# Performance work log

Hardware: AMD Instinct MI355X
Metric: run time of the kernel (lower is better)

Reference implementation:

```python
import jax, jax.numpy as jnp
import numpy as np

BETA = 0.25            # commitment loss weight
ENT_RATIO = 0.1        # entropy regularization weight
ENT_TEMP = 0.01        # entropy loss temperature
EPS = 1e-5


def setup_inputs() -> dict:
    key = jax.random.key(0)
    k1, k2 = jax.random.split(key)
    z = jax.random.normal(k1, (32, 8, 16, 16), dtype=jnp.float32)       # [B, e_dim, H, W]
    codebook = jax.random.normal(k2, (16384, 8), dtype=jnp.float32)     # [K, e_dim]
    return {"z": z, "codebook": codebook}


def _entropy_loss(affinity):
    # affinity: [N, K] = -distances; torch divides by temperature in-place
    flat = affinity / ENT_TEMP
    probs = jax.nn.softmax(flat, axis=-1)
    log_probs = jax.nn.log_softmax(flat + EPS, axis=-1)
    avg_probs = jnp.mean(probs, axis=0)                                  # [K]
    avg_entropy = -jnp.sum(avg_probs * jnp.log(avg_probs + EPS))
    sample_entropy = -jnp.mean(jnp.sum(probs * log_probs, axis=-1))
    return sample_entropy - avg_entropy


def reference(z, codebook):
    B, C, H, W = z.shape
    sg = jax.lax.stop_gradient
    # [B,C,H,W] -> [N, e_dim]
    zf = jnp.transpose(z, (0, 2, 3, 1)).reshape(-1, C)
    # squared euclidean distances: ||z||^2 + ||e||^2 - 2 z e^T  -> [N, K]
    d = (jnp.sum(zf * zf, axis=1, keepdims=True)
         + jnp.sum(codebook * codebook, axis=1)[None, :]
         - 2.0 * jnp.einsum('nd,kd->nk', zf, codebook))
    idx = jnp.argmin(d, axis=1)                                          # [N]
    zq_f = codebook[idx]                                                 # [N, e_dim] gather
    # VQ losses (codebook + beta * commitment) and entropy regularization
    vq_loss = jnp.mean((zq_f - sg(zf)) ** 2)
    commit_loss = BETA * jnp.mean((sg(zq_f) - zf) ** 2)
    ent_loss = ENT_RATIO * _entropy_loss(-d)
    loss = vq_loss + commit_loss + ent_loss
    # straight-through estimator
    zq_f = zf + sg(zq_f - zf)
    z_q = jnp.transpose(zq_f.reshape(B, H, W, C), (0, 3, 1, 2))
    return z_q, loss, idx.reshape(B, H, W)
```

## Files before the change

kernel.cpp:

```cpp
#include <hip/hip_runtime.h>
#include <math.h>


#define KCODES 16384
#define CAP 192

__device__ __forceinline__ float dot8s(const float (&z)[8], float4 c0,
                                       float4 c1, float b) {
    float a = fmaf(z[0], c0.x, b);
    a = fmaf(z[1], c0.y, a);
    a = fmaf(z[2], c0.z, a);
    a = fmaf(z[3], c0.w, a);
    a = fmaf(z[4], c1.x, a);
    a = fmaf(z[5], c1.y, a);
    a = fmaf(z[6], c1.z, a);
    a = fmaf(z[7], c1.w, a);
    return a;
}

__global__ __launch_bounds__(256) void prep_cb(const float* __restrict__ cb,
                                               float* __restrict__ bk,
                                               float* __restrict__ avgp,
                                               int* __restrict__ flag,
                                               float* __restrict__ scal) {
    int k = blockIdx.x * 256 + threadIdx.x;
    const float4* c4 = (const float4*)cb;
    float4 c0 = c4[2 * k], c1 = c4[2 * k + 1];
    float nrm = c0.x * c0.x + c0.y * c0.y + c0.z * c0.z + c0.w * c0.w
              + c1.x * c1.x + c1.y * c1.y + c1.z * c1.z + c1.w * c1.w;
    bk[k] = -100.0f * nrm;
    avgp[k] = 0.0f;
    if (k < 8192) flag[k] = 0;
    if (k < 8)    scal[k] = 0.0f;
}

__global__ __launch_bounds__(256, 2) void pass1(
    const float* __restrict__ z, const float* __restrict__ cb,
    const float* __restrict__ bk, float* __restrict__ mrow,
    int* __restrict__ flag, float* __restrict__ out_zq,
    float* __restrict__ out_idx, float* __restrict__ scal,
    float* __restrict__ avgp)
{
    __shared__ float wfb[16][CAP];
    __shared__ int   wkb[16][CAP];
    __shared__ int   cnt[16];
    __shared__ float redSq[4], redEnt[4];

    const int wave = threadIdx.x >> 6;
    const int lane = threadIdx.x & 63;
    const int w4 = wave * 4;
    const int row0 = blockIdx.x * 16 + w4;

    float zr[4][8];
#pragma unroll
    for (int r = 0; r < 4; ++r) {
        int row = row0 + r;
        const float* p = z + (row >> 8) * 2048 + (row & 255);
#pragma unroll
        for (int c = 0; c < 8; ++c) zr[r][c] = 200.0f * p[c * 256];
    }
    if (lane < 4) cnt[w4 + lane] = 0;
    __syncthreads();

    const float4* c4 = (const float4*)cb;
    float m[4], mt[4];
#pragma unroll
    for (int r = 0; r < 4; ++r) m[r] = -3.4e38f;

#pragma unroll
    for (int j = 0; j < 8; ++j) {
        int k = lane + 64 * j;
        float4 c0 = c4[2 * k], c1 = c4[2 * k + 1];
        float b = bk[k];
#pragma unroll
        for (int r = 0; r < 4; ++r) m[r] = fmaxf(m[r], dot8s(zr[r], c0, c1, b));
    }
#pragma unroll
    for (int off = 32; off; off >>= 1) {
#pragma unroll
        for (int r = 0; r < 4; ++r) m[r] = fmaxf(m[r], __shfl_xor(m[r], off));
    }
#pragma unroll
    for (int r = 0; r < 4; ++r) mt[r] = m[r] - 87.0f;

    float4 A0[4], A1[4]; float Ab[4];
    float4 B0[4], B1[4]; float Bb[4];

    auto loadA = [&](int bat) {
#pragma unroll
        for (int jj = 0; jj < 4; ++jj) {
            int k = lane + bat * 256 + 64 * jj;
            A0[jj] = c4[2 * k]; A1[jj] = c4[2 * k + 1]; Ab[jj] = bk[k];
        }
    };
    auto loadB = [&](int bat) {
#pragma unroll
        for (int jj = 0; jj < 4; ++jj) {
            int k = lane + bat * 256 + 64 * jj;
            B0[jj] = c4[2 * k]; B1[jj] = c4[2 * k + 1]; Bb[jj] = bk[k];
        }
    };
    auto comp = [&](int bat, const float4 (&P0)[4], const float4 (&P1)[4],
                    const float (&PB)[4]) {
#pragma unroll
        for (int jj = 0; jj < 4; ++jj) {
            float f0 = dot8s(zr[0], P0[jj], P1[jj], PB[jj]);
            float f1 = dot8s(zr[1], P0[jj], P1[jj], PB[jj]);
            float f2 = dot8s(zr[2], P0[jj], P1[jj], PB[jj]);
            float f3 = dot8s(zr[3], P0[jj], P1[jj], PB[jj]);
            bool h0 = f0 > mt[0], h1 = f1 > mt[1];
            bool h2 = f2 > mt[2], h3 = f3 > mt[3];
            if (__any(h0 | h1 | h2 | h3)) {
                int k = lane + bat * 256 + 64 * jj;
                if (h0) { m[0] = fmaxf(m[0], f0); mt[0] = m[0] - 87.0f;
                    int s_ = atomicAdd(&cnt[w4 + 0], 1);
                    if (s_ < CAP) { wfb[w4 + 0][s_] = f0; wkb[w4 + 0][s_] = k; } }
                if (h1) { m[1] = fmaxf(m[1], f1); mt[1] = m[1] - 87.0f;
                    int s_ = atomicAdd(&cnt[w4 + 1], 1);
                    if (s_ < CAP) { wfb[w4 + 1][s_] = f1; wkb[w4 + 1][s_] = k; } }
                if (h2) { m[2] = fmaxf(m[2], f2); mt[2] = m[2] - 87.0f;
                    int s_ = atomicAdd(&cnt[w4 + 2], 1);
                    if (s_ < CAP) { wfb[w4 + 2][s_] = f2; wkb[w4 + 2][s_] = k; } }
                if (h3) { m[3] = fmaxf(m[3], f3); mt[3] = m[3] - 87.0f;
                    int s_ = atomicAdd(&cnt[w4 + 3], 1);
                    if (s_ < CAP) { wfb[w4 + 3][s_] = f3; wkb[w4 + 3][s_] = k; } }
            }
        }
    };

    loadA(0);
    for (int t = 0; t < 8; ++t) {
#pragma unroll
        for (int s = 0; s < 4; ++s) {
            const int b0 = t * 8 + s * 2;
            loadB((b0 + 1) & 63);
            comp(b0, A0, A1, Ab);
            loadA((b0 + 2) & 63);
            comp(b0 + 1, B0, B1, Bb);
        }
#pragma unroll
        for (int off = 32; off; off >>= 1) {
#pragma unroll
            for (int r = 0; r < 4; ++r)
                m[r] = fmaxf(m[r], __shfl_xor(m[r], off));
        }
#pragma unroll
        for (int r = 0; r < 4; ++r) mt[r] = m[r] - 87.0f;
    }
    __syncthreads();

    float entAcc = 0.0f, sqAcc = 0.0f;
#pragma unroll
    for (int r = 0; r < 4; ++r) {
        const int br = w4 + r;
        const int row = row0 + r;
        const float mm = m[r];
        int c = cnt[br];
        if (c > CAP) {
            if (lane == 0) { flag[row] = 1; mrow[row] = mm; }
            continue;
        }
        float sl = 0.0f, tl = 0.0f;
        int kmin = 0x7fffffff;
        for (int i = lane; i < c; i += 64) {
            float x = wfb[br][i] - mm;
            float e = 0.0f;
            if (x > -87.0f) {
                e = __expf(x);
                sl += e;
                tl = fmaf(x, e, tl);
                if (x == 0.0f) kmin = min(kmin, wkb[br][i]);
            }
            wfb[br][i] = e;
        }
#pragma unroll
        for (int off = 32; off; off >>= 1) {
            sl += __shfl_xor(sl, off);
            tl += __shfl_xor(tl, off);
            kmin = min(kmin, __shfl_xor(kmin, off));
        }
        float rs = 1.0f / sl;
        for (int i = lane; i < c; i += 64) {
            float e = wfb[br][i];
            if (e != 0.0f) atomicAdd(&avgp[wkb[br][i]], e * rs);
        }
        if (lane == 0) {
            entAcc += tl * rs - logf(sl);
            out_idx[row] = (float)kmin;
            float4 q0 = c4[2 * kmin], q1 = c4[2 * kmin + 1];
            float qv[8] = {q0.x, q0.y, q0.z, q0.w, q1.x, q1.y, q1.z, q1.w};
            int bb = row >> 8, hw = row & 255;
            const float* zraw = z + bb * 2048 + hw;
            float* o = out_zq + bb * 2048 + hw;
#pragma unroll
            for (int ch = 0; ch < 8; ++ch) {
                float raw = zraw[ch * 256];
                o[ch * 256] = qv[ch];
                float dq = qv[ch] - raw;
                sqAcc += dq * dq;
            }
        }
    }
    if (lane == 0) { redSq[wave] = sqAcc; redEnt[wave] = entAcc; }
    __syncthreads();
    if (threadIdx.x == 0) {
        atomicAdd(&scal[0], redSq[0] + redSq[1] + redSq[2] + redSq[3]);
        atomicAdd(&scal[1], redEnt[0] + redEnt[1] + redEnt[2] + redEnt[3]);
    }
}

__global__ __launch_bounds__(256) void fixup(
    const float* __restrict__ z, const float* __restrict__ cb,
    const float* __restrict__ bk, const float* __restrict__ mrow,
    const int* __restrict__ flag, float* __restrict__ avgp,
    float* __restrict__ out_zq, float* __restrict__ out_idx,
    float* __restrict__ scal)
{
    int n = blockIdx.x * 256 + threadIdx.x;
    if (n >= 8192 || flag[n] == 0) return;
    float zraw[8], zs[8];
    int bb = n >> 8, hw = n & 255;
#pragma unroll
    for (int c = 0; c < 8; ++c) {
        zraw[c] = z[bb * 2048 + c * 256 + hw];
        zs[c] = 200.0f * zraw[c];
    }
    const float4* c4 = (const float4*)cb;
    float m = mrow[n];
    float s = 0.0f, t = 0.0f;
    int kmin = 0x7fffffff;
    for (int k = 0; k < KCODES; ++k) {
        float f = dot8s(zs, c4[2 * k], c4[2 * k + 1], bk[k]);
        float x = f - m;
        if (x > -87.0f) {
            float e = __expf(x);
            s += e; t = fmaf(x, e, t);
            if (x == 0.0f) kmin = min(kmin, k);
        }
    }
    float rs = 1.0f / s;
    for (int k = 0; k < KCODES; ++k) {
        float f = dot8s(zs, c4[2 * k], c4[2 * k + 1], bk[k]);
        float x = f - m;
        if (x > -87.0f) atomicAdd(&avgp[k], __expf(x) * rs);
    }
    out_idx[n] = (float)kmin;
    float sq = 0.0f;
#pragma unroll
    for (int c = 0; c < 8; ++c) {
        float q = cb[kmin * 8 + c];
        out_zq[bb * 2048 + c * 256 + hw] = q;
        float dq = q - zraw[c];
        sq += dq * dq;
    }
    atomicAdd(&scal[0], sq);
    atomicAdd(&scal[1], t * rs - logf(s));
}

__global__ __launch_bounds__(256) void finalize(
    const float* __restrict__ avgp, const float* __restrict__ scal,
    float* __restrict__ out_loss)
{
    float acc = 0.0f;
    for (int k = threadIdx.x; k < KCODES; k += 256) {
        float avg = avgp[k] * (1.0f / 8192.0f);
        acc += avg * logf(avg + 1e-5f);
    }
#pragma unroll
    for (int off = 32; off > 0; off >>= 1) acc += __shfl_xor(acc, off);
    __shared__ float red[4];
    int wave = threadIdx.x >> 6, lane = threadIdx.x & 63;
    if (lane == 0) red[wave] = acc;
    __syncthreads();
    if (threadIdx.x == 0) {
        float T = red[0] + red[1] + red[2] + red[3];
        float loss = 1.25f * (scal[0] * (1.0f / 65536.0f))
                   + 0.1f * (T - scal[1] * (1.0f / 8192.0f));
        out_loss[0] = loss;
    }
}

extern "C" void kernel_launch(void* const* d_in, const int* in_sizes, int n_in,
                              void* d_out, int out_size, void* d_ws, size_t ws_size,
                              hipStream_t stream) {
    const float* z  = (const float*)d_in[0];
    const float* cb = (const float*)d_in[1];
    float* out = (float*)d_out;
    float* ws  = (float*)d_ws;

    float* bk   = ws;
    float* avgp = ws + 16384;
    float* scal = ws + 32768;
    int*   flag = (int*)(ws + 32776);
    float* mrow = ws + 40968;

    float* out_zq   = out;
    float* out_loss = out + 65536;
    float* out_idx  = out + 65537;

    prep_cb <<<64,  256, 0, stream>>>(cb, bk, avgp, flag, scal);
    pass1   <<<512, 256, 0, stream>>>(z, cb, bk, mrow, flag, out_zq, out_idx,
                                      scal, avgp);
    fixup   <<<32,  256, 0, stream>>>(z, cb, bk, mrow, flag, avgp, out_zq,
                                      out_idx, scal);
    finalize<<<1,   256, 0, stream>>>(avgp, scal, out_loss);
}
```

Measured before the change: 153.4 us.

## Fold overflow fixup into pass1 and widen codebook batch prefetch

Removes the separate fixup kernel and its flag/mrow workspace. Rows whose candidate buffer overflows, or that find no exact-max match, now redo the full softmax pass over all codes at wave level inside pass1. Each batch loads 8 codes per lane instead of 4, the batch loops are no longer unrolled, and the counter initialization moves to the first 16 threads. This drops one kernel launch and a serial per-thread fallback, at the cost of more registers, a possible occupancy drop, and wave-level divergence when overflow happens.

New measurement: 154.2 us. No clear change (+0.5%).

```diff
diff --git a/kernel.cpp b/kernel.cpp
--- a/kernel.cpp
+++ b/kernel.cpp
@@ -21,7 +21,6 @@
 __global__ __launch_bounds__(256) void prep_cb(const float* __restrict__ cb,
                                                float* __restrict__ bk,
                                                float* __restrict__ avgp,
-                                               int* __restrict__ flag,
                                                float* __restrict__ scal) {
     int k = blockIdx.x * 256 + threadIdx.x;
     const float4* c4 = (const float4*)cb;
@@ -30,14 +29,12 @@
               + c1.x * c1.x + c1.y * c1.y + c1.z * c1.z + c1.w * c1.w;
     bk[k] = -100.0f * nrm;
     avgp[k] = 0.0f;
-    if (k < 8192) flag[k] = 0;
-    if (k < 8)    scal[k] = 0.0f;
+    if (k < 8) scal[k] = 0.0f;
 }
 
 __global__ __launch_bounds__(256, 2) void pass1(
     const float* __restrict__ z, const float* __restrict__ cb,
-    const float* __restrict__ bk, float* __restrict__ mrow,
-    int* __restrict__ flag, float* __restrict__ out_zq,
+    const float* __restrict__ bk, float* __restrict__ out_zq,
     float* __restrict__ out_idx, float* __restrict__ scal,
     float* __restrict__ avgp)
 {
@@ -59,7 +56,7 @@
 #pragma unroll
         for (int c = 0; c < 8; ++c) zr[r][c] = 200.0f * p[c * 256];
     }
-    if (lane < 4) cnt[w4 + lane] = 0;
+    if (threadIdx.x < 16) cnt[threadIdx.x] = 0;
     __syncthreads();
 
     const float4* c4 = (const float4*)cb;
@@ -83,27 +80,27 @@
 #pragma unroll
     for (int r = 0; r < 4; ++r) mt[r] = m[r] - 87.0f;
 
-    float4 A0[4], A1[4]; float Ab[4];
-    float4 B0[4], B1[4]; float Bb[4];
+    float4 A0[8], A1[8]; float Ab[8];
+    float4 B0[8], B1[8]; float Bb[8];
 
     auto loadA = [&](int bat) {
 #pragma unroll
-        for (int jj = 0; jj < 4; ++jj) {
-            int k = lane + bat * 256 + 64 * jj;
+        for (int jj = 0; jj < 8; ++jj) {
+            int k = lane + bat * 512 + 64 * jj;
             A0[jj] = c4[2 * k]; A1[jj] = c4[2 * k + 1]; Ab[jj] = bk[k];
         }
     };
     auto loadB = [&](int bat) {
 #pragma unroll
-        for (int jj = 0; jj < 4; ++jj) {
-            int k = lane + bat * 256 + 64 * jj;
+        for (int jj = 0; jj < 8; ++jj) {
+            int k = lane + bat * 512 + 64 * jj;
             B0[jj] = c4[2 * k]; B1[jj] = c4[2 * k + 1]; Bb[jj] = bk[k];
         }
     };
-    auto comp = [&](int bat, const float4 (&P0)[4], const float4 (&P1)[4],
-                    const float (&PB)[4]) {
-#pragma unroll
-        for (int jj = 0; jj < 4; ++jj) {
+    auto comp = [&](int bat, const float4 (&P0)[8], const float4 (&P1)[8],
+                    const float (&PB)[8]) {
+#pragma unroll
+        for (int jj = 0; jj < 8; ++jj) {
             float f0 = dot8s(zr[0], P0[jj], P1[jj], PB[jj]);
             float f1 = dot8s(zr[1], P0[jj], P1[jj], PB[jj]);
             float f2 = dot8s(zr[2], P0[jj], P1[jj], PB[jj]);
@@ -111,7 +108,7 @@
             bool h0 = f0 > mt[0], h1 = f1 > mt[1];
             bool h2 = f2 > mt[2], h3 = f3 > mt[3];
             if (__any(h0 | h1 | h2 | h3)) {
-                int k = lane + bat * 256 + 64 * jj;
+                int k = lane + bat * 512 + 64 * jj;
                 if (h0) { m[0] = fmaxf(m[0], f0); mt[0] = m[0] - 87.0f;
                     int s_ = atomicAdd(&cnt[w4 + 0], 1);
                     if (s_ < CAP) { wfb[w4 + 0][s_] = f0; wkb[w4 + 0][s_] = k; } }
@@ -129,13 +126,14 @@
     };
 
     loadA(0);
+#pragma unroll 1
     for (int t = 0; t < 8; ++t) {
-#pragma unroll
-        for (int s = 0; s < 4; ++s) {
-            const int b0 = t * 8 + s * 2;
-            loadB((b0 + 1) & 63);
+#pragma unroll 1
+        for (int s = 0; s < 2; ++s) {
+            const int b0 = t * 4 + s * 2;
+            loadB(b0 + 1);
             comp(b0, A0, A1, Ab);
-            loadA((b0 + 2) & 63);
+            loadA((b0 + 2) & 31);
             comp(b0 + 1, B0, B1, Bb);
         }
 #pragma unroll
@@ -155,36 +153,66 @@
         const int br = w4 + r;
         const int row = row0 + r;
         const float mm = m[r];
-        int c = cnt[br];
-        if (c > CAP) {
-            if (lane == 0) { flag[row] = 1; mrow[row] = mm; }
-            continue;
-        }
+        const int c = cnt[br];
+
         float sl = 0.0f, tl = 0.0f;
         int kmin = 0x7fffffff;
-        for (int i = lane; i < c; i += 64) {
-            float x = wfb[br][i] - mm;
-            float e = 0.0f;
-            if (x > -87.0f) {
-                e = __expf(x);
-                sl += e;
-                tl = fmaf(x, e, tl);
-                if (x == 0.0f) kmin = min(kmin, wkb[br][i]);
-            }
-            wfb[br][i] = e;
-        }
-#pragma unroll
-        for (int off = 32; off; off >>= 1) {
-            sl += __shfl_xor(sl, off);
-            tl += __shfl_xor(tl, off);
-            kmin = min(kmin, __shfl_xor(kmin, off));
-        }
-        float rs = 1.0f / sl;
-        for (int i = lane; i < c; i += 64) {
-            float e = wfb[br][i];
-            if (e != 0.0f) atomicAdd(&avgp[wkb[br][i]], e * rs);
-        }
+        bool ok = (c <= CAP);
+
+        if (ok) {
+            for (int i = lane; i < c; i += 64) {
+                float x = wfb[br][i] - mm;
+                float e = 0.0f;
+                if (x > -87.0f) {
+                    e = __expf(x);
+                    sl += e;
+                    tl = fmaf(x, e, tl);
+                    if (x == 0.0f) kmin = min(kmin, wkb[br][i]);
+                }
+                wfb[br][i] = e;
+            }
+#pragma unroll
+            for (int off = 32; off; off >>= 1) {
+                sl += __shfl_xor(sl, off);
+                tl += __shfl_xor(tl, off);
+                kmin = min(kmin, __shfl_xor(kmin, off));
+            }
+            ok = (kmin != 0x7fffffff);
+        }
+
+        if (!ok) {
+            sl = 0.0f; tl = 0.0f; kmin = 0x7fffffff;
+            for (int k = lane; k < KCODES; k += 64) {
+                float f = dot8s(zr[r], c4[2 * k], c4[2 * k + 1], bk[k]);
+                float x = f - mm;
+                if (x > -87.0f) {
+                    float e = __expf(x);
+                    sl += e; tl = fmaf(x, e, tl);
+                    if (x == 0.0f) kmin = min(kmin, k);
+                }
+            }
+#pragma unroll
+            for (int off = 32; off; off >>= 1) {
+                sl += __shfl_xor(sl, off);
+                tl += __shfl_xor(tl, off);
+                kmin = min(kmin, __shfl_xor(kmin, off));
+            }
+            float rs = 1.0f / sl;
+            for (int k = lane; k < KCODES; k += 64) {
+                float f = dot8s(zr[r], c4[2 * k], c4[2 * k + 1], bk[k]);
+                float x = f - mm;
+                if (x > -87.0f) atomicAdd(&avgp[k], __expf(x) * rs);
+            }
+        } else {
+            float rs = 1.0f / sl;
+            for (int i = lane; i < c; i += 64) {
+                float e = wfb[br][i];
+                if (e != 0.0f) atomicAdd(&avgp[wkb[br][i]], e * rs);
+            }
+        }
+
         if (lane == 0) {
+            float rs = 1.0f / sl;
             entAcc += tl * rs - logf(sl);
             out_idx[row] = (float)kmin;
             float4 q0 = c4[2 * kmin], q1 = c4[2 * kmin + 1];
@@ -207,54 +235,6 @@
         atomicAdd(&scal[0], redSq[0] + redSq[1] + redSq[2] + redSq[3]);
         atomicAdd(&scal[1], redEnt[0] + redEnt[1] + redEnt[2] + redEnt[3]);
     }
-}
-
-__global__ __launch_bounds__(256) void fixup(
-    const float* __restrict__ z, const float* __restrict__ cb,
-    const float* __restrict__ bk, const float* __restrict__ mrow,
-    const int* __restrict__ flag, float* __restrict__ avgp,
-    float* __restrict__ out_zq, float* __restrict__ out_idx,
-    float* __restrict__ scal)
-{
-    int n = blockIdx.x * 256 + threadIdx.x;
-    if (n >= 8192 || flag[n] == 0) return;
-    float zraw[8], zs[8];
-    int bb = n >> 8, hw = n & 255;
-#pragma unroll
-    for (int c = 0; c < 8; ++c) {
-        zraw[c] = z[bb * 2048 + c * 256 + hw];
-        zs[c] = 200.0f * zraw[c];
-    }
-    const float4* c4 = (const float4*)cb;
-    float m = mrow[n];
-    float s = 0.0f, t = 0.0f;
-    int kmin = 0x7fffffff;
-    for (int k = 0; k < KCODES; ++k) {
-        float f = dot8s(zs, c4[2 * k], c4[2 * k + 1], bk[k]);
-        float x = f - m;
-        if (x > -87.0f) {
-            float e = __expf(x);
-            s += e; t = fmaf(x, e, t);
-            if (x == 0.0f) kmin = min(kmin, k);
-        }
-    }
-    float rs = 1.0f / s;
-    for (int k = 0; k < KCODES; ++k) {
-        float f = dot8s(zs, c4[2 * k], c4[2 * k + 1], bk[k]);
-        float x = f - m;
-        if (x > -87.0f) atomicAdd(&avgp[k], __expf(x) * rs);
-    }
-    out_idx[n] = (float)kmin;
-    float sq = 0.0f;
-#pragma unroll
-    for (int c = 0; c < 8; ++c) {
-        float q = cb[kmin * 8 + c];
-        out_zq[bb * 2048 + c * 256 + hw] = q;
-        float dq = q - zraw[c];
-        sq += dq * dq;
-    }
-    atomicAdd(&scal[0], sq);
-    atomicAdd(&scal[1], t * rs - logf(s));
 }
 
 __global__ __launch_bounds__(256) void finalize(
@@ -291,17 +271,12 @@
     float* bk   = ws;
     float* avgp = ws + 16384;
     float* scal = ws + 32768;
-    int*   flag = (int*)(ws + 32776);
-    float* mrow = ws + 40968;
 
     float* out_zq   = out;
     float* out_loss = out + 65536;
     float* out_idx  = out + 65537;
 
-    prep_cb <<<64,  256, 0, stream>>>(cb, bk, avgp, flag, scal);
-    pass1   <<<512, 256, 0, stream>>>(z, cb, bk, mrow, flag, out_zq, out_idx,
-                                      scal, avgp);
-    fixup   <<<32,  256, 0, stream>>>(z, cb, bk, mrow, flag, avgp, out_zq,
-                                      out_idx, scal);
+    prep_cb <<<64,  256, 0, stream>>>(cb, bk, avgp, scal);
+    pass1   <<<512, 256, 0, stream>>>(z, cb, bk, out_zq, out_idx, scal, avgp);
     finalize<<<1,   256, 0, stream>>>(avgp, scal, out_loss);
 }
```
